# Optimization experiments

Hardware: AMD Instinct MI355X
Metric: run time of the kernel (lower is better)

Reference implementation:

```python
import jax, jax.numpy as jnp
import numpy as np

B = 2
D = 256
NH = 8
DH = D // NH
LV = 4
NP_ = 4
NL = 6
DFF = 1024
SHAPES = [(112, 112), (56, 56), (28, 28), (14, 14)]
S = sum(h * w for h, w in SHAPES)


def setup_inputs() -> dict:
    key = jax.random.key(0)
    ks = iter(jax.random.split(key, 64))
    d = {}
    for i, (h, w) in enumerate(SHAPES):
        d[f"src{i}"] = jax.random.normal(next(ks), (B, D, h, w), jnp.float32)
        d[f"pos{i}"] = jax.random.normal(next(ks), (B, D, h, w), jnp.float32)

    def W(*shape, scale=0.02):
        return jax.random.normal(next(ks), shape, jnp.float32) * scale

    d["level_embed"] = W(LV, D, scale=1.0)
    d["off_w"] = W(NL, D, NH * LV * NP_ * 2)
    d["off_b"] = W(NL, NH * LV * NP_ * 2, scale=0.5)
    d["aw_w"] = W(NL, D, NH * LV * NP_)
    d["aw_b"] = jnp.zeros((NL, NH * LV * NP_), jnp.float32)
    d["val_w"] = W(NL, D, D)
    d["val_b"] = jnp.zeros((NL, D), jnp.float32)
    d["out_w"] = W(NL, D, D)
    d["out_b"] = jnp.zeros((NL, D), jnp.float32)
    d["ln1_s"] = jnp.ones((NL, D), jnp.float32)
    d["ln1_b"] = jnp.zeros((NL, D), jnp.float32)
    d["ff1_w"] = W(NL, D, DFF)
    d["ff1_b"] = jnp.zeros((NL, DFF), jnp.float32)
    d["ff2_w"] = W(NL, DFF, D)
    d["ff2_b"] = jnp.zeros((NL, D), jnp.float32)
    d["ln2_s"] = jnp.ones((NL, D), jnp.float32)
    d["ln2_b"] = jnp.zeros((NL, D), jnp.float32)
    return d


def _ln(x, s, b):
    m = jnp.mean(x, -1, keepdims=True)
    v = jnp.mean((x - m) ** 2, -1, keepdims=True)
    return (x - m) / jnp.sqrt(v + 1e-5) * s + b


def _bilinear(v, loc, Hl, Wl):
    # v: [N, DH, Hl, Wl]; loc: [N, Q, P, 2] in [0,1] (grid_sample align_corners=False, zero padding)
    N, Dh = v.shape[0], v.shape[1]
    Q, P = loc.shape[1], loc.shape[2]
    x = loc[..., 0] * Wl - 0.5
    y = loc[..., 1] * Hl - 0.5
    x0f = jnp.floor(x)
    y0f = jnp.floor(y)
    lx = x - x0f
    ly = y - y0f
    x0 = x0f.astype(jnp.int32)
    y0 = y0f.astype(jnp.int32)
    vf = v.reshape(N, Dh, Hl * Wl)

    def g(xi, yi):
        valid = (xi >= 0) & (xi < Wl) & (yi >= 0) & (yi < Hl)
        idx = (jnp.clip(yi, 0, Hl - 1) * Wl + jnp.clip(xi, 0, Wl - 1)).reshape(N, Q * P)
        out = jnp.take_along_axis(vf, idx[:, None, :], axis=2).reshape(N, Dh, Q, P)
        return out * valid[:, None].astype(v.dtype)

    w00 = ((1 - lx) * (1 - ly))[:, None]
    w10 = (lx * (1 - ly))[:, None]
    w01 = ((1 - lx) * ly)[:, None]
    w11 = (lx * ly)[:, None]
    return g(x0, y0) * w00 + g(x0 + 1, y0) * w10 + g(x0, y0 + 1) * w01 + g(x0 + 1, y0 + 1) * w11


def _ms_deform_attn(value, loc, attn):
    # value [B,S,NH,DH], loc [B,S,NH,LV,P,2], attn [B,S,NH,LV,P]
    out = jnp.zeros((B * NH, DH, S), value.dtype)
    s0 = 0
    for l, (Hl, Wl) in enumerate(SHAPES):
        vl = value[:, s0:s0 + Hl * Wl].reshape(B, Hl, Wl, NH, DH)
        vl = vl.transpose(0, 3, 4, 1, 2).reshape(B * NH, DH, Hl, Wl)
        ll = loc[:, :, :, l].transpose(0, 2, 1, 3, 4).reshape(B * NH, S, NP_, 2)
        al = attn[:, :, :, l].transpose(0, 2, 1, 3).reshape(B * NH, S, NP_)[:, None]
        out = out + (_bilinear(vl, ll, Hl, Wl) * al).sum(-1)
        s0 += Hl * Wl
    return out.reshape(B, NH * DH, S).transpose(0, 2, 1)


def _forward(srcs, poss, level_embed, off_w, off_b, aw_w, aw_b, val_w, val_b,
             out_w, out_b, ln1_s, ln1_b, ff1_w, ff1_b, ff2_w, ff2_b, ln2_s, ln2_b):
    src = jnp.concatenate([s.reshape(B, D, -1).transpose(0, 2, 1) for s in srcs], 1)
    pos = jnp.concatenate(
        [p.reshape(B, D, -1).transpose(0, 2, 1) + level_embed[i][None, None] for i, p in enumerate(poss)], 1)
    # reference points: padding masks are all-False => valid_ratios == 1
    refs = []
    for (Hl, Wl) in SHAPES:
        gy, gx = jnp.meshgrid((jnp.arange(Hl) + 0.5) / Hl, (jnp.arange(Wl) + 0.5) / Wl, indexing="ij")
        refs.append(jnp.stack([gx.ravel(), gy.ravel()], -1))
    ref = jnp.concatenate(refs, 0)  # [S, 2]
    normalizer = jnp.array([[w, h] for (h, w) in SHAPES], jnp.float32)  # [LV, 2] = (W, H)
    x = src
    for i in range(NL):
        q = x + pos
        off = (q @ off_w[i] + off_b[i]).reshape(B, S, NH, LV, NP_, 2)
        aw = jax.nn.softmax((q @ aw_w[i] + aw_b[i]).reshape(B, S, NH, LV * NP_), -1)
        aw = aw.reshape(B, S, NH, LV, NP_)
        val = (x @ val_w[i] + val_b[i]).reshape(B, S, NH, DH)
        loc = ref[None, :, None, None, None, :] + off / normalizer[None, None, None, :, None, :]
        attn_out = _ms_deform_attn(val, loc, aw) @ out_w[i] + out_b[i]
        x = _ln(x + attn_out, ln1_s[i], ln1_b[i])
        ff = jax.nn.relu(x @ ff1_w[i] + ff1_b[i]) @ ff2_w[i] + ff2_b[i]
        x = _ln(x + ff, ln2_s[i], ln2_b[i])
    return x


def reference(src0, src1, src2, src3, pos0, pos1, pos2, pos3, level_embed,
              off_w, off_b, aw_w, aw_b, val_w, val_b, out_w, out_b,
              ln1_s, ln1_b, ff1_w, ff1_b, ff2_w, ff2_b, ln2_s, ln2_b):
    memory = _forward([src0, src1, src2, src3], [pos0, pos1, pos2, pos3], level_embed,
                      off_w, off_b, aw_w, aw_b, val_w, val_b, out_w, out_b,
                      ln1_s, ln1_b, ff1_w, ff1_b, ff2_w, ff2_b, ln2_s, ln2_b)
    spatial_shapes = jnp.array(SHAPES, jnp.int32)
    level_start_index = jnp.concatenate(
        [jnp.zeros((1,), jnp.int32), jnp.cumsum(spatial_shapes.prod(1))[:-1].astype(jnp.int32)])
    return memory, spatial_shapes, level_start_index
```

## Files before the change

### kernel.cpp

```cpp
#include <hip/hip_runtime.h>


constexpr int kB  = 2;
constexpr int kD  = 256;
constexpr int kNH = 8;
constexpr int kLV = 4;
constexpr int kNP = 4;
constexpr int kNL = 6;
constexpr int kDFF = 1024;
constexpr int kS  = 16660;
constexpr int kM  = kB * kS;
constexpr int kMp = 33408;
constexpr int kMT64 = kMp / 64;
constexpr int kPERS = 512;

typedef short bf16x8 __attribute__((ext_vector_type(8)));
typedef float f32x4  __attribute__((ext_vector_type(4)));

__device__ __forceinline__ unsigned short f2bf(float x) {
  union { float f; unsigned int u; } v; v.f = x;
  unsigned int r = v.u + 0x7FFFu + ((v.u >> 16) & 1u);
  return (unsigned short)(r >> 16);
}
__device__ __forceinline__ float bf2f(unsigned short u) {
  union { unsigned int u; float f; } v; v.u = ((unsigned int)u) << 16;
  return v.f;
}
__device__ __forceinline__ float bflo(unsigned int u) {
  union { unsigned int u; float f; } v; v.u = u << 16;
  return v.f;
}
__device__ __forceinline__ float bfhi(unsigned int u) {
  union { unsigned int u; float f; } v; v.u = u & 0xFFFF0000u;
  return v.f;
}

#define GLOAD_LDS16(gp, lp)                                                    \
  __builtin_amdgcn_global_load_lds(                                            \
      (const __attribute__((address_space(1))) void*)(gp),                     \
      (__attribute__((address_space(3))) void*)(lp), 16, 0, 0)

#define SBARRIER() asm volatile("s_barrier" ::: "memory")

__global__ __launch_bounds__(256) void build_xpos_k(
    const float* __restrict__ src, const float* __restrict__ pos,
    const float* __restrict__ lemb, unsigned short* __restrict__ posbf,
    unsigned short* __restrict__ xbf, unsigned short* __restrict__ qbf,
    int HW, int s0, int lvl)
{
  __shared__ float ts[32][33];
  __shared__ float tp[32][33];
  const int b  = blockIdx.z;
  const int p0 = blockIdx.x * 32, d0 = blockIdx.y * 32;
  const int tx = threadIdx.x, ty = threadIdx.y;
  for (int dd = ty; dd < 32; dd += 8) {
    int p = p0 + tx;
    if (p < HW) {
      size_t idx = ((size_t)b * kD + (d0 + dd)) * (size_t)HW + p;
      ts[dd][tx] = src[idx];
      tp[dd][tx] = pos[idx];
    }
  }
  __syncthreads();
  for (int pp = ty; pp < 32; pp += 8) {
    int p = p0 + pp, d = d0 + tx;
    if (p < HW) {
      size_t o = ((size_t)b * kS + (s0 + p)) * (size_t)kD + d;
      float x = ts[tx][pp];
      float pv = tp[tx][pp] + lemb[lvl * kD + d];
      posbf[o] = f2bf(pv);
      xbf[o] = f2bf(x);
      qbf[o] = f2bf(x + pv);
    }
  }
}

__global__ __launch_bounds__(256) void wconv_k(
    const float* __restrict__ W, unsigned short* __restrict__ Wt,
    int K, int N, int rowoff, int rowstotal)
{
  __shared__ float t[32][33];
  const int l = blockIdx.z;
  const int n0 = blockIdx.x * 32, k0 = blockIdx.y * 32;
  const int tx = threadIdx.x & 31, ty = threadIdx.x >> 5;
  const float* Wl = W + (size_t)l * K * N;
  unsigned short* Wtl = Wt + (size_t)l * rowstotal * K;
  for (int kk = ty; kk < 32; kk += 8)
    t[kk][tx] = Wl[(size_t)(k0 + kk) * N + n0 + tx];
  __syncthreads();
  for (int nn = ty; nn < 32; nn += 8)
    Wtl[(size_t)(rowoff + n0 + nn) * K + k0 + tx] = f2bf(t[tx][nn]);
}

__global__ __launch_bounds__(256) void biaspack_k(
    const float* __restrict__ ob, const float* __restrict__ ab,
    float* __restrict__ qb)
{
  int i = blockIdx.x * 256 + threadIdx.x;
  if (i >= kNL * 384) return;
  int l = i / 384, c = i - l * 384;
  qb[i] = (c < 256) ? ob[l * 256 + c] : ab[l * 128 + (c - 256)];
}

__global__ __launch_bounds__(256) void refxy_k(float* __restrict__ ref)
{
  int s = blockIdx.x * 256 + threadIdx.x;
  if (s >= kS) return;
  int ls, side;
  if (s < 12544)      { ls = s;         side = 112; }
  else if (s < 15680) { ls = s - 12544; side = 56;  }
  else if (s < 16464) { ls = s - 15680; side = 28;  }
  else                { ls = s - 16464; side = 14;  }
  const float inv = 1.0f / (float)side;
  ref[s * 2 + 0] = ((ls % side) + 0.5f) * inv;
  ref[s * 2 + 1] = ((ls / side) + 0.5f) * inv;
}

template<int RELU, int OUTBF>
__global__ __launch_bounds__(256) void hgemm64_k(
    const unsigned short* __restrict__ A, const unsigned short* __restrict__ Bt,
    const float* __restrict__ bias, void* __restrict__ Cout, int N, int K)
{
  __shared__ unsigned short As[2][64 * 32];
  __shared__ unsigned short Bs[2][128 * 32];
  const int tid = threadIdx.x;
  const int bm = blockIdx.y * 64;
  const int bn = blockIdx.x * 128;
  const int lane = tid & 63;
  const int wave = tid >> 6;
  const int wr = (wave >> 1) * 32, wc = (wave & 1) * 64;
  const int l15 = lane & 15, l4 = lane >> 4;

  f32x4 acc[2][4] = {};

  const unsigned short* A0 = A + (size_t)(bm + (tid >> 2)) * K + ((tid & 3) << 3);
  const int cb1 = 256 + tid;
  const unsigned short* B0 = Bt + (size_t)(bn + (tid >> 2)) * K + ((tid & 3) << 3);
  const unsigned short* B1 = Bt + (size_t)(bn + (cb1 >> 2)) * K + ((cb1 & 3) << 3);

#define STAGE64(buf, k0)                                                       \
  do {                                                                         \
    GLOAD_LDS16(A0 + (k0), (char*)As[buf] + tid * 16);                         \
    GLOAD_LDS16(B0 + (k0), (char*)Bs[buf] + tid * 16);                         \
    GLOAD_LDS16(B1 + (k0), (char*)Bs[buf] + cb1 * 16);                         \
  } while (0)

  const int nt = K >> 5;
  STAGE64(0, 0);
  STAGE64(1, 32);
  for (int k = 0; k < nt; ++k) {
    if (k + 1 < nt) asm volatile("s_waitcnt vmcnt(3)" ::: "memory");
    else            asm volatile("s_waitcnt vmcnt(0)" ::: "memory");
    SBARRIER();
    __builtin_amdgcn_sched_barrier(0);
    const int cur = k & 1;
    bf16x8 af[2], bfr[4];
#pragma unroll
    for (int m = 0; m < 2; ++m)
      af[m] = *(const bf16x8*)&As[cur][(wr + m * 16 + l15) * 32 + l4 * 8];
#pragma unroll
    for (int n = 0; n < 4; ++n)
      bfr[n] = *(const bf16x8*)&Bs[cur][(wc + n * 16 + l15) * 32 + l4 * 8];
#pragma unroll
    for (int m = 0; m < 2; ++m)
#pragma unroll
      for (int n = 0; n < 4; ++n)
        acc[m][n] = __builtin_amdgcn_mfma_f32_16x16x32_bf16(
            af[m], bfr[n], acc[m][n], 0, 0, 0);
    SBARRIER();
    if (k + 2 < nt) STAGE64(cur, (k + 2) * 32);
  }
#undef STAGE64

#pragma unroll
  for (int n = 0; n < 4; ++n) {
    const int col = bn + wc + n * 16 + l15;
    const float bv = bias[col];
#pragma unroll
    for (int m = 0; m < 2; ++m) {
#pragma unroll
      for (int j = 0; j < 4; ++j) {
        const int row = bm + wr + m * 16 + l4 * 4 + j;
        float v = acc[m][n][j] + bv;
        if (RELU) v = fmaxf(v, 0.f);
        if (OUTBF)
          ((unsigned short*)Cout)[(size_t)row * N + col] = f2bf(v);
        else
          ((float*)Cout)[(size_t)row * N + col] = v;
      }
    }
  }
}

__global__ __launch_bounds__(256) void qvgemm_k(
    const unsigned short* __restrict__ Aq, const unsigned short* __restrict__ Ax,
    const unsigned short* __restrict__ Bq, const unsigned short* __restrict__ Bv,
    const float* __restrict__ biasq, const float* __restrict__ biasv,
    _Float16* __restrict__ Cq, unsigned short* __restrict__ Cv)
{
  constexpr int K = 256;
  __shared__ unsigned short As[2][64 * 32];
  __shared__ unsigned short Bs[2][128 * 32];
  const int tid = threadIdx.x;
  const int bx = blockIdx.x;
  const bool isv = bx >= 3;
  const int bn = (isv ? bx - 3 : bx) * 128;
  const int bm = blockIdx.y * 64;
  const unsigned short* A  = isv ? Ax : Aq;
  const unsigned short* Bt = isv ? Bv : Bq;
  const float* bias = isv ? biasv : biasq;
  const int lane = tid & 63;
  const int wave = tid >> 6;
  const int wr = (wave >> 1) * 32, wc = (wave & 1) * 64;
  const int l15 = lane & 15, l4 = lane >> 4;

  f32x4 acc[2][4] = {};

  const unsigned short* A0 = A + (size_t)(bm + (tid >> 2)) * K + ((tid & 3) << 3);
  const int cb1 = 256 + tid;
  const unsigned short* B0 = Bt + (size_t)(bn + (tid >> 2)) * K + ((tid & 3) << 3);
  const unsigned short* B1 = Bt + (size_t)(bn + (cb1 >> 2)) * K + ((cb1 & 3) << 3);

#define STAGEQV(buf, k0)                                                       \
  do {                                                                         \
    GLOAD_LDS16(A0 + (k0), (char*)As[buf] + tid * 16);                         \
    GLOAD_LDS16(B0 + (k0), (char*)Bs[buf] + tid * 16);                         \
    GLOAD_LDS16(B1 + (k0), (char*)Bs[buf] + cb1 * 16);                         \
  } while (0)

  const int nt = K >> 5;
  STAGEQV(0, 0);
  STAGEQV(1, 32);
  for (int k = 0; k < nt; ++k) {
    if (k + 1 < nt) asm volatile("s_waitcnt vmcnt(3)" ::: "memory");
    else            asm volatile("s_waitcnt vmcnt(0)" ::: "memory");
    SBARRIER();
    __builtin_amdgcn_sched_barrier(0);
    const int cur = k & 1;
    bf16x8 af[2], bfr[4];
#pragma unroll
    for (int m = 0; m < 2; ++m)
      af[m] = *(const bf16x8*)&As[cur][(wr + m * 16 + l15) * 32 + l4 * 8];
#pragma unroll
    for (int n = 0; n < 4; ++n)
      bfr[n] = *(const bf16x8*)&Bs[cur][(wc + n * 16 + l15) * 32 + l4 * 8];
#pragma unroll
    for (int m = 0; m < 2; ++m)
#pragma unroll
      for (int n = 0; n < 4; ++n)
        acc[m][n] = __builtin_amdgcn_mfma_f32_16x16x32_bf16(
            af[m], bfr[n], acc[m][n], 0, 0, 0);
    SBARRIER();
    if (k + 2 < nt) STAGEQV(cur, (k + 2) * 32);
  }
#undef STAGEQV

#pragma unroll
  for (int n = 0; n < 4; ++n) {
    const int col = bn + wc + n * 16 + l15;
    const float bv = bias[col];
#pragma unroll
    for (int m = 0; m < 2; ++m) {
#pragma unroll
      for (int j = 0; j < 4; ++j) {
        const int row = bm + wr + m * 16 + l4 * 4 + j;
        float v = acc[m][n][j] + bv;
        if (isv)
          Cv[(size_t)row * 256 + col] = f2bf(v);
        else
          Cq[(size_t)row * 384 + col] = (_Float16)v;
      }
    }
  }
}

template<int WQ, int OUTDST>
__global__ __launch_bounds__(512) void hgemmln_k(
    const unsigned short* __restrict__ A, const unsigned short* __restrict__ Bt,
    const float* __restrict__ bias, const unsigned short* __restrict__ Rsd,
    const float* __restrict__ g, const float* __restrict__ beta,
    const unsigned short* __restrict__ posbf, float* __restrict__ yout,
    unsigned short* __restrict__ xbf, unsigned short* __restrict__ qbf, int K)
{
  __shared__ unsigned short As[2][64 * 32];
  __shared__ unsigned short Bs[2][256 * 32];
  __shared__ float ssum[64][5];
  __shared__ float ssq[64][5];
  const int tid = threadIdx.x;
  const int lane = tid & 63;
  const int wave = tid >> 6;
  const int wm = wave >> 2;
  const int wn = wave & 3;
  const int wc = wn * 64;
  const int l15 = lane & 15, l4 = lane >> 4;

  const unsigned short* Bq0 = Bt + (size_t)(tid >> 2) * K + ((tid & 3) << 3);
  const unsigned short* Bq1 = Bt + (size_t)(128 + (tid >> 2)) * K + ((tid & 3) << 3);

  float bv[4], gv[4], btv[4];
#pragma unroll
  for (int n = 0; n < 4; ++n) {
    const int col = wc + n * 16 + l15;
    bv[n] = bias[col];
    gv[n] = g[col];
    btv[n] = beta[col];
  }

  for (int tile = blockIdx.x; tile < kMT64; tile += kPERS) {
    const int bm = tile * 64;
    const unsigned short* Aq =
        A + (size_t)(bm + (tid >> 2)) * K + ((tid & 3) << 3);

    f32x4 acc[2][4] = {};

#define STAGE_LN(buf, k0)                                                      \
  do {                                                                         \
    if (tid < 256) GLOAD_LDS16(Aq + (k0), (char*)As[buf] + tid * 16);          \
    GLOAD_LDS16(Bq0 + (k0), (char*)Bs[buf] + tid * 16);                        \
    GLOAD_LDS16(Bq1 + (k0), (char*)Bs[buf] + (512 + tid) * 16);                \
  } while (0)

    const int nt = K >> 5;
    STAGE_LN(0, 0);
    STAGE_LN(1, 32);
    for (int k = 0; k < nt; ++k) {
      if (k + 1 < nt) {
        if (wave < 4) asm volatile("s_waitcnt vmcnt(3)" ::: "memory");
        else          asm volatile("s_waitcnt vmcnt(2)" ::: "memory");
      } else {
        asm volatile("s_waitcnt vmcnt(0)" ::: "memory");
      }
      SBARRIER();
      __builtin_amdgcn_sched_barrier(0);
      const int cur = k & 1;
      bf16x8 af[2], bfr[4];
#pragma unroll
      for (int m = 0; m < 2; ++m)
        af[m] = *(const bf16x8*)&As[cur][(wm * 32 + m * 16 + l15) * 32 + l4 * 8];
#pragma unroll
      for (int n = 0; n < 4; ++n)
        bfr[n] = *(const bf16x8*)&Bs[cur][(wc + n * 16 + l15) * 32 + l4 * 8];
#pragma unroll
      for (int m = 0; m < 2; ++m)
#pragma unroll
        for (int n = 0; n < 4; ++n)
          acc[m][n] = __builtin_amdgcn_mfma_f32_16x16x32_bf16(
              af[m], bfr[n], acc[m][n], 0, 0, 0);
      SBARRIER();
      if (k + 2 < nt) STAGE_LN(cur, (k + 2) * 32);
    }
#undef STAGE_LN

#pragma unroll
    for (int m = 0; m < 2; ++m) {
#pragma unroll
      for (int j = 0; j < 4; ++j) {
        const int row = bm + wm * 32 + m * 16 + l4 * 4 + j;
#pragma unroll
        for (int n = 0; n < 4; ++n)
          acc[m][n][j] +=
              bv[n] + bf2f(Rsd[(size_t)row * kD + wc + n * 16 + l15]);
      }
    }
#pragma unroll
    for (int m = 0; m < 2; ++m) {
#pragma unroll
      for (int j = 0; j < 4; ++j) {
        float s = acc[m][0][j] + acc[m][1][j] + acc[m][2][j] + acc[m][3][j];
        float q = acc[m][0][j] * acc[m][0][j] + acc[m][1][j] * acc[m][1][j] +
                  acc[m][2][j] * acc[m][2][j] + acc[m][3][j] * acc[m][3][j];
#pragma unroll
        for (int d2 = 1; d2 < 16; d2 <<= 1) {
          s += __shfl_xor(s, d2, 64);
          q += __shfl_xor(q, d2, 64);
        }
        if (l15 == 0) {
          const int r = wm * 32 + m * 16 + l4 * 4 + j;
          ssum[r][wn] = s;
          ssq[r][wn] = q;
        }
      }
    }
    __syncthreads();
#pragma unroll
    for (int m = 0; m < 2; ++m) {
#pragma unroll
      for (int j = 0; j < 4; ++j) {
        const int r = wm * 32 + m * 16 + l4 * 4 + j;
        const int row = bm + r;
        const float mean = (ssum[r][0] + ssum[r][1] + ssum[r][2] + ssum[r][3]) *
                           (1.0f / kD);
        const float var = (ssq[r][0] + ssq[r][1] + ssq[r][2] + ssq[r][3]) *
                          (1.0f / kD) - mean * mean;
        const float rstd = rsqrtf(var + 1e-5f);
        if (row < kM) {
#pragma unroll
          for (int n = 0; n < 4; ++n) {
            const int col = wc + n * 16 + l15;
            const float y = (acc[m][n][j] - mean) * rstd * gv[n] + btv[n];
            const size_t o = (size_t)row * kD + col;
            if (OUTDST) {
              yout[o] = y;
            } else {
              xbf[o] = f2bf(y);
              if (WQ) qbf[o] = f2bf(y + bf2f(posbf[o]));
            }
          }
        }
      }
    }
    asm volatile("s_waitcnt vmcnt(0)" ::: "memory");
    SBARRIER();
  }
}

__global__ __launch_bounds__(256) void msdeform_k(
    const unsigned short* __restrict__ val, const _Float16* __restrict__ qout,
    const float* __restrict__ ref, unsigned short* __restrict__ outbf)
{
  __shared__ int   sIdx[4][8][128];
  __shared__ float sW[4][8][128];
  const int bid = blockIdx.x;
  const int xcd = bid & 7;
  const int jj  = bid >> 3;
  const int wg  = (xcd < 5 ? xcd * 521 : 5 * 521 + (xcd - 5) * 520) + jj;
  const int bs0 = wg * 8;
  const int tid = threadIdx.x;

#pragma unroll
  for (int it = 0; it < 4; ++it) {
    const int item = tid + it * 256;
    const int q = item >> 7;
    const int t = item & 127;
    const int bs = bs0 + q;
    const int b = bs / kS, s = bs - b * kS;
    const int l = (t & 15) >> 2;

    const float logit = (float)qout[(size_t)bs * 384 + 256 + t];
    float mx = logit;
#pragma unroll
    for (int d2 = 1; d2 < 16; d2 <<= 1) mx = fmaxf(mx, __shfl_xor(mx, d2, 64));
    float e = __expf(logit - mx);
    float sm = e;
#pragma unroll
    for (int d2 = 1; d2 < 16; d2 <<= 1) sm += __shfl_xor(sm, d2, 64);
    const float a = e / sm;

    const float rfx = ref[s * 2 + 0];
    const float rfy = ref[s * 2 + 1];
    const int side  = 112 >> l;
    const int start = (l >= 1 ? 12544 : 0) + (l >= 2 ? 3136 : 0) + (l >= 3 ? 784 : 0);
    const float ox = (float)qout[(size_t)bs * 384 + t * 2 + 0];
    const float oy = (float)qout[(size_t)bs * 384 + t * 2 + 1];
    const float xx = fmaf(rfx, (float)side, ox) - 0.5f;
    const float yy = fmaf(rfy, (float)side, oy) - 0.5f;
    const float xf = floorf(xx), yf = floorf(yy);
    const float lx = xx - xf, ly = yy - yf;
    const int x0 = (int)xf, y0 = (int)yf;
    const float w00 = (1.f - lx) * (1.f - ly) * a, w10 = lx * (1.f - ly) * a;
    const float w01 = (1.f - lx) * ly * a,         w11 = lx * ly * a;
    const bool xv0 = (unsigned)x0 < (unsigned)side, xv1 = (unsigned)(x0 + 1) < (unsigned)side;
    const bool yv0 = (unsigned)y0 < (unsigned)side, yv1 = (unsigned)(y0 + 1) < (unsigned)side;
    const int cx0 = min(max(x0, 0), side - 1), cx1 = min(max(x0 + 1, 0), side - 1);
    const int cy0 = min(max(y0, 0), side - 1), cy1 = min(max(y0 + 1, 0), side - 1);
    const int rowbase = b * kS + start;
    const int t2 = (t & 15) * 8 + (t >> 4);
    sIdx[0][q][t2] = (rowbase + cy0 * side + cx0) << 9;
    sIdx[1][q][t2] = (rowbase + cy0 * side + cx1) << 9;
    sIdx[2][q][t2] = (rowbase + cy1 * side + cx0) << 9;
    sIdx[3][q][t2] = (rowbase + cy1 * side + cx1) << 9;
    sW[0][q][t2] = (xv0 && yv0) ? w00 : 0.f;
    sW[1][q][t2] = (xv1 && yv0) ? w10 : 0.f;
    sW[2][q][t2] = (xv0 && yv1) ? w01 : 0.f;
    sW[3][q][t2] = (xv1 && yv1) ? w11 : 0.f;
  }
  __syncthreads();

  const int q  = tid >> 5;
  const int h  = (tid >> 2) & 7;
  const int l4 = tid & 3;
  const char* vbase = (const char*)val + h * 64 + l4 * 16;

  float a0 = 0.f, a1 = 0.f, a2 = 0.f, a3 = 0.f;
  float a4 = 0.f, a5 = 0.f, a6 = 0.f, a7 = 0.f;
#pragma unroll
  for (int sp = 0; sp < 16; ++sp) {
    const int t2 = sp * 8 + h;
#pragma unroll
    for (int c = 0; c < 4; ++c) {
      const int off = sIdx[c][q][t2];
      const float w = sW[c][q][t2];
      const uint4 v = *(const uint4*)(vbase + off);
      a0 = fmaf(w, bflo(v.x), a0); a1 = fmaf(w, bfhi(v.x), a1);
      a2 = fmaf(w, bflo(v.y), a2); a3 = fmaf(w, bfhi(v.y), a3);
      a4 = fmaf(w, bflo(v.z), a4); a5 = fmaf(w, bfhi(v.z), a5);
      a6 = fmaf(w, bflo(v.w), a6); a7 = fmaf(w, bfhi(v.w), a7);
    }
  }
  bf16x8 o;
  o[0] = (short)f2bf(a0); o[1] = (short)f2bf(a1);
  o[2] = (short)f2bf(a2); o[3] = (short)f2bf(a3);
  o[4] = (short)f2bf(a4); o[5] = (short)f2bf(a5);
  o[6] = (short)f2bf(a6); o[7] = (short)f2bf(a7);
  *(bf16x8*)(outbf + (size_t)(bs0 + q) * 256 + h * 32 + l4 * 8) = o;
}

__global__ void tail_k(float* __restrict__ out)
{
  if (threadIdx.x == 0) {
    const size_t n = (size_t)kM * kD;
    out[n + 0] = 112.f; out[n + 1] = 112.f;
    out[n + 2] = 56.f;  out[n + 3] = 56.f;
    out[n + 4] = 28.f;  out[n + 5] = 28.f;
    out[n + 6] = 14.f;  out[n + 7] = 14.f;
    out[n + 8] = 0.f;   out[n + 9] = 12544.f;
    out[n + 10] = 15680.f; out[n + 11] = 16464.f;
  }
}

extern "C" void kernel_launch(void* const* d_in, const int* in_sizes, int n_in,
                              void* d_out, int out_size, void* d_ws, size_t ws_size,
                              hipStream_t stream)
{
  const float* src[4] = {(const float*)d_in[0], (const float*)d_in[2],
                         (const float*)d_in[4], (const float*)d_in[6]};
  const float* pos[4] = {(const float*)d_in[1], (const float*)d_in[3],
                         (const float*)d_in[5], (const float*)d_in[7]};
  const float* lemb  = (const float*)d_in[8];
  const float* off_w = (const float*)d_in[9];
  const float* off_b = (const float*)d_in[10];
  const float* aw_w  = (const float*)d_in[11];
  const float* aw_b  = (const float*)d_in[12];
  const float* val_w = (const float*)d_in[13];
  const float* val_b = (const float*)d_in[14];
  const float* out_w = (const float*)d_in[15];
  const float* out_b = (const float*)d_in[16];
  const float* ln1_s = (const float*)d_in[17];
  const float* ln1_b = (const float*)d_in[18];
  const float* ff1_w = (const float*)d_in[19];
  const float* ff1_b = (const float*)d_in[20];
  const float* ff2_w = (const float*)d_in[21];
  const float* ff2_b = (const float*)d_in[22];
  const float* ln2_s = (const float*)d_in[23];
  const float* ln2_b = (const float*)d_in[24];

  const size_t SZ = (size_t)kMp * kD;
  float* ws   = (float*)d_ws;
  _Float16* qoutH = (_Float16*)(ws + SZ);
  unsigned short* valbf = (unsigned short*)(ws + SZ + (3 * SZ) / 4);
  unsigned short* attbf = valbf + SZ;
  unsigned short* ffbf  = (unsigned short*)(ws + SZ);
  unsigned short* posbf = (unsigned short*)(ws + 3 * SZ);
  unsigned short* qbf   = posbf + SZ;
  unsigned short* xbf   = qbf + SZ;
  unsigned short* wts   = (unsigned short*)(ws + 4 * SZ + SZ / 2);
  unsigned short* qwT  = wts;
  unsigned short* valT = qwT + kNL * 384 * 256;
  unsigned short* outT = valT + kNL * 256 * 256;
  unsigned short* ff1T = outT + kNL * 256 * 256;
  unsigned short* ff2T = ff1T + kNL * 1024 * 256;
  float* qbias = (float*)(ff2T + kNL * 256 * 1024);
  float* reftab = qbias + kNL * 384;

  wconv_k<<<dim3(256 / 32, 256 / 32, kNL), 256, 0, stream>>>(off_w, qwT, 256, 256, 0, 384);
  wconv_k<<<dim3(128 / 32, 256 / 32, kNL), 256, 0, stream>>>(aw_w,  qwT, 256, 128, 256, 384);
  wconv_k<<<dim3(256 / 32, 256 / 32, kNL), 256, 0, stream>>>(val_w, valT, 256, 256, 0, 256);
  wconv_k<<<dim3(256 / 32, 256 / 32, kNL), 256, 0, stream>>>(out_w, outT, 256, 256, 0, 256);
  wconv_k<<<dim3(1024 / 32, 256 / 32, kNL), 256, 0, stream>>>(ff1_w, ff1T, 256, 1024, 0, 1024);
  wconv_k<<<dim3(256 / 32, 1024 / 32, kNL), 256, 0, stream>>>(ff2_w, ff2T, 1024, 256, 0, 256);
  biaspack_k<<<(kNL * 384 + 255) / 256, 256, 0, stream>>>(off_b, aw_b, qbias);
  refxy_k<<<(kS + 255) / 256, 256, 0, stream>>>(reftab);

  const int sides[4]  = {112, 56, 28, 14};
  const int starts[4] = {0, 12544, 15680, 16464};
  for (int l = 0; l < 4; ++l) {
    int HW = sides[l] * sides[l];
    dim3 g((HW + 31) / 32, kD / 32, kB);
    build_xpos_k<<<g, dim3(32, 8), 0, stream>>>(src[l], pos[l], lemb, posbf,
                                                xbf, qbf, HW, starts[l], l);
  }

  const dim3 blk(256);
  for (int i = 0; i < kNL; ++i) {
    qvgemm_k<<<dim3(5, kMT64), blk, 0, stream>>>(
        qbf, xbf, qwT + (size_t)i * 384 * 256, valT + (size_t)i * 256 * 256,
        qbias + i * 384, val_b + i * 256, qoutH, valbf);
    msdeform_k<<<kM / 8, blk, 0, stream>>>(valbf, qoutH, reftab, attbf);
    hgemmln_k<0, 0><<<kPERS, 512, 0, stream>>>(
        attbf, outT + (size_t)i * 256 * 256, out_b + i * 256, xbf,
        ln1_s + i * kD, ln1_b + i * kD, nullptr, nullptr, xbf, nullptr, 256);
    hgemm64_k<1, 1><<<dim3(8, kMT64), blk, 0, stream>>>(
        xbf, ff1T + (size_t)i * 1024 * 256, ff1_b + i * 1024, ffbf, 1024, 256);
    if (i < kNL - 1) {
      hgemmln_k<1, 0><<<kPERS, 512, 0, stream>>>(
          ffbf, ff2T + (size_t)i * 256 * 1024, ff2_b + i * 256, xbf,
          ln2_s + i * kD, ln2_b + i * kD, posbf, nullptr, xbf, qbf, 1024);
    } else {
      hgemmln_k<0, 1><<<kPERS, 512, 0, stream>>>(
          ffbf, ff2T + (size_t)i * 256 * 1024, ff2_b + i * 256, xbf,
          ln2_s + i * kD, ln2_b + i * kD, nullptr, (float*)d_out, nullptr,
          nullptr, 1024);
    }
  }

  tail_k<<<1, 64, 0, stream>>>((float*)d_out);
}
```

Baseline: 1.285 ms.

## Fuse FFN up-projection, ReLU, down-projection and LayerNorm into one kernel

Replaces the separate FF1 GEMM (which wrote a bf16 hidden buffer of M×1024) and the FF2+LayerNorm persistent kernel with a single fused FFN kernel per 64-row tile. Each block streams 64-column chunks of W1, computes the ReLU hidden chunk into LDS, and immediately accumulates it against the matching W2 slice, so the hidden activation never goes to global memory. The residual, bias and LayerNorm are applied in the epilogue. The cost is that each block re-reads the full W1 and W2 weights, uses larger LDS and has more barriers per chunk, which may lower occupancy.

```diff
diff --git a/kernel.cpp b/kernel.cpp
--- a/kernel.cpp
+++ b/kernel.cpp
@@ -114,82 +114,6 @@
   const float inv = 1.0f / (float)side;
   ref[s * 2 + 0] = ((ls % side) + 0.5f) * inv;
   ref[s * 2 + 1] = ((ls / side) + 0.5f) * inv;
-}
-
-template<int RELU, int OUTBF>
-__global__ __launch_bounds__(256) void hgemm64_k(
-    const unsigned short* __restrict__ A, const unsigned short* __restrict__ Bt,
-    const float* __restrict__ bias, void* __restrict__ Cout, int N, int K)
-{
-  __shared__ unsigned short As[2][64 * 32];
-  __shared__ unsigned short Bs[2][128 * 32];
-  const int tid = threadIdx.x;
-  const int bm = blockIdx.y * 64;
-  const int bn = blockIdx.x * 128;
-  const int lane = tid & 63;
-  const int wave = tid >> 6;
-  const int wr = (wave >> 1) * 32, wc = (wave & 1) * 64;
-  const int l15 = lane & 15, l4 = lane >> 4;
-
-  f32x4 acc[2][4] = {};
-
-  const unsigned short* A0 = A + (size_t)(bm + (tid >> 2)) * K + ((tid & 3) << 3);
-  const int cb1 = 256 + tid;
-  const unsigned short* B0 = Bt + (size_t)(bn + (tid >> 2)) * K + ((tid & 3) << 3);
-  const unsigned short* B1 = Bt + (size_t)(bn + (cb1 >> 2)) * K + ((cb1 & 3) << 3);
-
-#define STAGE64(buf, k0)                                                       \
-  do {                                                                         \
-    GLOAD_LDS16(A0 + (k0), (char*)As[buf] + tid * 16);                         \
-    GLOAD_LDS16(B0 + (k0), (char*)Bs[buf] + tid * 16);                         \
-    GLOAD_LDS16(B1 + (k0), (char*)Bs[buf] + cb1 * 16);                         \
-  } while (0)
-
-  const int nt = K >> 5;
-  STAGE64(0, 0);
-  STAGE64(1, 32);
-  for (int k = 0; k < nt; ++k) {
-    if (k + 1 < nt) asm volatile("s_waitcnt vmcnt(3)" ::: "memory");
-    else            asm volatile("s_waitcnt vmcnt(0)" ::: "memory");
-    SBARRIER();
-    __builtin_amdgcn_sched_barrier(0);
-    const int cur = k & 1;
-    bf16x8 af[2], bfr[4];
-#pragma unroll
-    for (int m = 0; m < 2; ++m)
-      af[m] = *(const bf16x8*)&As[cur][(wr + m * 16 + l15) * 32 + l4 * 8];
-#pragma unroll
-    for (int n = 0; n < 4; ++n)
-      bfr[n] = *(const bf16x8*)&Bs[cur][(wc + n * 16 + l15) * 32 + l4 * 8];
-#pragma unroll
-    for (int m = 0; m < 2; ++m)
-#pragma unroll
-      for (int n = 0; n < 4; ++n)
-        acc[m][n] = __builtin_amdgcn_mfma_f32_16x16x32_bf16(
-            af[m], bfr[n], acc[m][n], 0, 0, 0);
-    SBARRIER();
-    if (k + 2 < nt) STAGE64(cur, (k + 2) * 32);
-  }
-#undef STAGE64
-
-#pragma unroll
-  for (int n = 0; n < 4; ++n) {
-    const int col = bn + wc + n * 16 + l15;
-    const float bv = bias[col];
-#pragma unroll
-    for (int m = 0; m < 2; ++m) {
-#pragma unroll
-      for (int j = 0; j < 4; ++j) {
-        const int row = bm + wr + m * 16 + l4 * 4 + j;
-        float v = acc[m][n][j] + bv;
-        if (RELU) v = fmaxf(v, 0.f);
-        if (OUTBF)
-          ((unsigned short*)Cout)[(size_t)row * N + col] = f2bf(v);
-        else
-          ((float*)Cout)[(size_t)row * N + col] = v;
-      }
-    }
-  }
 }
 
 __global__ __launch_bounds__(256) void qvgemm_k(
@@ -411,6 +335,190 @@
     }
     asm volatile("s_waitcnt vmcnt(0)" ::: "memory");
     SBARRIER();
+  }
+}
+
+template<int WQ, int OUTDST>
+__global__ __launch_bounds__(512) void ffn_k(
+    const unsigned short* __restrict__ xA,
+    const unsigned short* __restrict__ W1t,
+    const unsigned short* __restrict__ W2t,
+    const float* __restrict__ b1,
+    const float* __restrict__ b2,
+    const float* __restrict__ g, const float* __restrict__ beta,
+    const unsigned short* __restrict__ posbf, float* __restrict__ yout,
+    unsigned short* __restrict__ xbf, unsigned short* __restrict__ qbf)
+{
+  __shared__ unsigned short xs[8 * 64 * 32];
+  __shared__ unsigned short w1s[2][8 * 64 * 32];
+  __shared__ unsigned short w2s[2 * 256 * 32];
+  __shared__ unsigned short Ps[2 * 64 * 32];
+  __shared__ float b1s[1024];
+  __shared__ float ssum[64][5];
+  __shared__ float ssq[64][5];
+
+  const int tid = threadIdx.x;
+  const int bm = blockIdx.x * 64;
+  const int lane = tid & 63;
+  const int wave = tid >> 6;
+  const int wm = wave >> 2;
+  const int wn = wave & 3;
+  const int l15 = lane & 15, l4 = lane >> 4;
+
+  const int n6 = (tid >> 2) & 63;
+  const int n7 = tid >> 2;
+  const int kq = tid & 3;
+  const int sb = tid >> 8;
+
+  b1s[tid] = b1[tid];
+  b1s[tid + 512] = b1[tid + 512];
+
+#pragma unroll
+  for (int i = 0; i < 4; ++i) {
+    const int slab = i * 2 + sb;
+    GLOAD_LDS16(xA + (size_t)(bm + n6) * 256 + slab * 32 + kq * 8,
+                (char*)xs + slab * 4096 + n6 * 64 + kq * 16);
+    GLOAD_LDS16(W1t + (size_t)n6 * 256 + slab * 32 + kq * 8,
+                (char*)w1s[0] + slab * 4096 + n6 * 64 + kq * 16);
+  }
+
+  f32x4 acc[2][4] = {};
+
+  for (int cc = 0; cc < 16; ++cc) {
+    const int p = cc & 1;
+#pragma unroll
+    for (int s = 0; s < 2; ++s)
+#pragma unroll
+      for (int i = 0; i < 2; ++i)
+        GLOAD_LDS16(W2t + (size_t)(i * 128 + n7) * 1024 + cc * 64 + s * 32 + kq * 8,
+                    (char*)w2s + s * 16384 + (i * 128 + n7) * 64 + kq * 16);
+    if (cc + 1 < 16) {
+#pragma unroll
+      for (int i = 0; i < 4; ++i) {
+        const int slab = i * 2 + sb;
+        GLOAD_LDS16(W1t + (size_t)((cc + 1) * 64 + n6) * 256 + slab * 32 + kq * 8,
+                    (char*)w1s[p ^ 1] + slab * 4096 + n6 * 64 + kq * 16);
+      }
+      asm volatile("s_waitcnt vmcnt(8)" ::: "memory");
+    } else {
+      asm volatile("s_waitcnt vmcnt(4)" ::: "memory");
+    }
+    SBARRIER();
+    __builtin_amdgcn_sched_barrier(0);
+
+    f32x4 acc1[2] = {};
+#pragma unroll
+    for (int kk = 0; kk < 8; ++kk) {
+      bf16x8 a0 = *(const bf16x8*)((char*)xs + kk * 4096 + (wm * 32 + l15) * 64 + l4 * 16);
+      bf16x8 a1 = *(const bf16x8*)((char*)xs + kk * 4096 + (wm * 32 + 16 + l15) * 64 + l4 * 16);
+      bf16x8 b0 = *(const bf16x8*)((char*)w1s[p] + kk * 4096 + (wn * 16 + l15) * 64 + l4 * 16);
+      acc1[0] = __builtin_amdgcn_mfma_f32_16x16x32_bf16(a0, b0, acc1[0], 0, 0, 0);
+      acc1[1] = __builtin_amdgcn_mfma_f32_16x16x32_bf16(a1, b0, acc1[1], 0, 0, 0);
+    }
+    const float b1c = b1s[cc * 64 + wn * 16 + l15];
+    const int pcol = (wn >> 1) * 2048 + (wn & 1) * 16 + l15;
+#pragma unroll
+    for (int m = 0; m < 2; ++m)
+#pragma unroll
+      for (int j = 0; j < 4; ++j) {
+        const int row = wm * 32 + m * 16 + l4 * 4 + j;
+        float v = fmaxf(acc1[m][j] + b1c, 0.f);
+        Ps[pcol + row * 32] = f2bf(v);
+      }
+    asm volatile("s_waitcnt lgkmcnt(0)" ::: "memory");
+    if (cc + 1 < 16) asm volatile("s_waitcnt vmcnt(4)" ::: "memory");
+    else             asm volatile("s_waitcnt vmcnt(0)" ::: "memory");
+    SBARRIER();
+    __builtin_amdgcn_sched_barrier(0);
+
+#pragma unroll
+    for (int kk = 0; kk < 2; ++kk) {
+      bf16x8 a0 = *(const bf16x8*)((char*)Ps + kk * 4096 + (wm * 32 + l15) * 64 + l4 * 16);
+      bf16x8 a1 = *(const bf16x8*)((char*)Ps + kk * 4096 + (wm * 32 + 16 + l15) * 64 + l4 * 16);
+      bf16x8 w0 = *(const bf16x8*)((char*)w2s + kk * 16384 + (wn * 64 + 0 * 16 + l15) * 64 + l4 * 16);
+      bf16x8 w1 = *(const bf16x8*)((char*)w2s + kk * 16384 + (wn * 64 + 1 * 16 + l15) * 64 + l4 * 16);
+      bf16x8 w2 = *(const bf16x8*)((char*)w2s + kk * 16384 + (wn * 64 + 2 * 16 + l15) * 64 + l4 * 16);
+      bf16x8 w3 = *(const bf16x8*)((char*)w2s + kk * 16384 + (wn * 64 + 3 * 16 + l15) * 64 + l4 * 16);
+      acc[0][0] = __builtin_amdgcn_mfma_f32_16x16x32_bf16(a0, w0, acc[0][0], 0, 0, 0);
+      acc[1][0] = __builtin_amdgcn_mfma_f32_16x16x32_bf16(a1, w0, acc[1][0], 0, 0, 0);
+      acc[0][1] = __builtin_amdgcn_mfma_f32_16x16x32_bf16(a0, w1, acc[0][1], 0, 0, 0);
+      acc[1][1] = __builtin_amdgcn_mfma_f32_16x16x32_bf16(a1, w1, acc[1][1], 0, 0, 0);
+      acc[0][2] = __builtin_amdgcn_mfma_f32_16x16x32_bf16(a0, w2, acc[0][2], 0, 0, 0);
+      acc[1][2] = __builtin_amdgcn_mfma_f32_16x16x32_bf16(a1, w2, acc[1][2], 0, 0, 0);
+      acc[0][3] = __builtin_amdgcn_mfma_f32_16x16x32_bf16(a0, w3, acc[0][3], 0, 0, 0);
+      acc[1][3] = __builtin_amdgcn_mfma_f32_16x16x32_bf16(a1, w3, acc[1][3], 0, 0, 0);
+    }
+    SBARRIER();
+  }
+
+  const int wc = wn * 64;
+  float bv[4], gv[4], btv[4];
+#pragma unroll
+  for (int n = 0; n < 4; ++n) {
+    const int col = wc + n * 16 + l15;
+    bv[n] = b2[col];
+    gv[n] = g[col];
+    btv[n] = beta[col];
+  }
+#pragma unroll
+  for (int m = 0; m < 2; ++m) {
+#pragma unroll
+    for (int j = 0; j < 4; ++j) {
+      const int row = wm * 32 + m * 16 + l4 * 4 + j;
+#pragma unroll
+      for (int n = 0; n < 4; ++n) {
+        const int col = wc + n * 16 + l15;
+        const float rx = bf2f(xs[(col >> 5) * 2048 + row * 32 + (col & 31)]);
+        acc[m][n][j] += bv[n] + rx;
+      }
+    }
+  }
+#pragma unroll
+  for (int m = 0; m < 2; ++m) {
+#pragma unroll
+    for (int j = 0; j < 4; ++j) {
+      float s = acc[m][0][j] + acc[m][1][j] + acc[m][2][j] + acc[m][3][j];
+      float q = acc[m][0][j] * acc[m][0][j] + acc[m][1][j] * acc[m][1][j] +
+                acc[m][2][j] * acc[m][2][j] + acc[m][3][j] * acc[m][3][j];
+#pragma unroll
+      for (int d2 = 1; d2 < 16; d2 <<= 1) {
+        s += __shfl_xor(s, d2, 64);
+        q += __shfl_xor(q, d2, 64);
+      }
+      if (l15 == 0) {
+        const int r = wm * 32 + m * 16 + l4 * 4 + j;
+        ssum[r][wn] = s;
+        ssq[r][wn] = q;
+      }
+    }
+  }
+  __syncthreads();
+#pragma unroll
+  for (int m = 0; m < 2; ++m) {
+#pragma unroll
+    for (int j = 0; j < 4; ++j) {
+      const int r = wm * 32 + m * 16 + l4 * 4 + j;
+      const int row = bm + r;
+      const float mean = (ssum[r][0] + ssum[r][1] + ssum[r][2] + ssum[r][3]) *
+                         (1.0f / kD);
+      const float var = (ssq[r][0] + ssq[r][1] + ssq[r][2] + ssq[r][3]) *
+                        (1.0f / kD) - mean * mean;
+      const float rstd = rsqrtf(var + 1e-5f);
+      if (row < kM) {
+#pragma unroll
+        for (int n = 0; n < 4; ++n) {
+          const int col = wc + n * 16 + l15;
+          const float y = (acc[m][n][j] - mean) * rstd * gv[n] + btv[n];
+          const size_t o = (size_t)row * kD + col;
+          if (OUTDST) {
+            yout[o] = y;
+          } else {
+            xbf[o] = f2bf(y);
+            if (WQ) qbf[o] = f2bf(y + bf2f(posbf[o]));
+          }
+        }
+      }
+    }
   }
 }
 
@@ -549,7 +657,6 @@
   _Float16* qoutH = (_Float16*)(ws + SZ);
   unsigned short* valbf = (unsigned short*)(ws + SZ + (3 * SZ) / 4);
   unsigned short* attbf = valbf + SZ;
-  unsigned short* ffbf  = (unsigned short*)(ws + SZ);
   unsigned short* posbf = (unsigned short*)(ws + 3 * SZ);
   unsigned short* qbf   = posbf + SZ;
   unsigned short* xbf   = qbf + SZ;
@@ -589,17 +696,16 @@
     hgemmln_k<0, 0><<<kPERS, 512, 0, stream>>>(
         attbf, outT + (size_t)i * 256 * 256, out_b + i * 256, xbf,
         ln1_s + i * kD, ln1_b + i * kD, nullptr, nullptr, xbf, nullptr, 256);
-    hgemm64_k<1, 1><<<dim3(8, kMT64), blk, 0, stream>>>(
-        xbf, ff1T + (size_t)i * 1024 * 256, ff1_b + i * 1024, ffbf, 1024, 256);
     if (i < kNL - 1) {
-      hgemmln_k<1, 0><<<kPERS, 512, 0, stream>>>(
-          ffbf, ff2T + (size_t)i * 256 * 1024, ff2_b + i * 256, xbf,
-          ln2_s + i * kD, ln2_b + i * kD, posbf, nullptr, xbf, qbf, 1024);
+      ffn_k<1, 0><<<kMT64, 512, 0, stream>>>(
+          xbf, ff1T + (size_t)i * 1024 * 256, ff2T + (size_t)i * 256 * 1024,
+          ff1_b + i * 1024, ff2_b + i * 256, ln2_s + i * kD, ln2_b + i * kD,
+          posbf, nullptr, xbf, qbf);
     } else {
-      hgemmln_k<0, 1><<<kPERS, 512, 0, stream>>>(
-          ffbf, ff2T + (size_t)i * 256 * 1024, ff2_b + i * 256, xbf,
-          ln2_s + i * kD, ln2_b + i * kD, nullptr, (float*)d_out, nullptr,
-          nullptr, 1024);
+      ffn_k<0, 1><<<kMT64, 512, 0, stream>>>(
+          xbf, ff1T + (size_t)i * 1024 * 256, ff2T + (size_t)i * 256 * 1024,
+          ff1_b + i * 1024, ff2_b + i * 256, ln2_s + i * kD, ln2_b + i * kD,
+          nullptr, (float*)d_out, nullptr, nullptr);
     }
   }
 
```

New measurement: 1.407 ms. 1.1x slower.
